# Optimization experiments

Hardware: AMD Instinct MI355X
Metric: run time of the kernel (lower is better)

The kernel has to match this reference:

```python
import jax, jax.numpy as jnp
import numpy as np

M_BITS = 4            # mem_pot_bits
M_MASK = (1 << M_BITS) - 1
T_MASK = (1 << 4) - 1  # t_bits = 4
ALPHA = 0.5


def setup_inputs() -> dict:
    key = jax.random.key(0)
    ks = jax.random.split(key, 8)
    B, N_IN, N_OUT, M = 256, 4096, 4096, 1 << M_BITS
    return {
        "active_mask": jax.random.randint(ks[0], (B, N_IN), 0, 2, dtype=jnp.int32),
        "t": 7,
        "prev_neuron_id": jax.random.randint(ks[1], (N_IN,), 0, M, dtype=jnp.int32),
        "t_last": jnp.zeros((B,), jnp.int32),
        "mem_fict": jax.random.uniform(ks[2], (B, N_OUT), jnp.float32),
        "mem_phys": jax.random.randint(ks[3], (B, N_OUT), 0, M, dtype=jnp.int32),
        "accumulate_lut_delta": jnp.zeros((N_OUT, M), jnp.float32),
        "tau": jax.random.uniform(ks[4], (N_OUT,), jnp.float32),
        "v_th": jax.random.uniform(ks[5], (N_OUT,), jnp.float32),
        "syn_w": jax.random.uniform(ks[6], (N_IN, N_OUT), jnp.float32),
        "mem_map": jax.nn.sigmoid(jax.random.normal(ks[7], (N_OUT, M), jnp.float32)),
    }


def reference(active_mask, t, prev_neuron_id, t_last, mem_fict, mem_phys,
              accumulate_lut_delta, tau, v_th, syn_w, mem_map):
    # delta_t = (t - t_last) & t_bit_mask  (Python '&' binds looser than '-')
    delta_t = (t - t_last) & T_MASK                          # (B,)
    t_last_new = jnp.full_like(t_last, t)

    # masked matmul + exponential membrane decay
    weights_sum = active_mask.astype(jnp.float32) @ syn_w    # (B, N_out)
    decay = jnp.exp(-tau[None, :] * delta_t[:, None].astype(jnp.float32))
    mem_fict_new = mem_fict * decay + weights_sum

    # XOR tree-reduction over masked input ids == bitwise parity per bit.
    # Only the low M_BITS matter (result is masked by m_bit_mask afterwards).
    masked_ids = jnp.where(active_mask.astype(bool), prev_neuron_id[None, :], 0)
    shifts = jnp.arange(M_BITS, dtype=jnp.int32)
    bits = (masked_ids[:, :, None] >> shifts) & 1            # (B, N_in, M_BITS)
    parity = jnp.sum(bits, axis=1) & 1                       # (B, M_BITS)
    acc = jnp.sum(parity << shifts, axis=1)                  # (B,)

    # physical membrane update (all low-bit integer ops)
    mem_phys_new = (mem_phys ^ delta_t[:, None] ^ acc[:, None]) & M_MASK

    # LUT gather + threshold
    n_out = mem_map.shape[0]
    rows = jnp.broadcast_to(jnp.arange(n_out)[None, :], mem_phys_new.shape)
    v_map_vals = mem_map[rows, mem_phys_new]                 # (B, N_out)
    active_next = v_map_vals >= v_th[None, :]

    # scatter-add per-bucket LUT delta (alpha != 0 path)
    delta = ALPHA * (mem_phys_new.astype(jnp.float32) - v_map_vals)
    lut_new = accumulate_lut_delta.at[rows, mem_phys_new].add(delta)

    return active_next, mem_fict_new, mem_phys_new, lut_new, t_last_new
```

## Files before the change

### kernel.cpp

```cpp
#include <hip/hip_runtime.h>

typedef __attribute__((ext_vector_type(8))) short short8;
typedef __attribute__((ext_vector_type(4))) float f32x4;
typedef unsigned int u32;

#define N_IN  4096
#define N_OUT 4096
#define NBAT  256

#define OUT_ACT   0
#define OUT_FICT  1048576
#define OUT_PHYS  2097152
#define OUT_LUT   3145728
#define OUT_TLAST 3211264

#define WS_MASK   0
#define WS_PART   2097152
#define WS_DTF    (WS_PART + 16777216)
#define WS_DXA    (WS_DTF + 1024)

#define BM 128
#define BN 64
#define BK 64
#define SPLITK 4
#define KCHUNK (N_IN / SPLITK)
#define NTK (KCHUNK / BK)

__device__ __forceinline__ unsigned f2bf(float f) {
  unsigned u = __float_as_uint(f);
  return (u + 0x7FFFu + ((u >> 16) & 1u)) >> 16;
}

__device__ __forceinline__ void gload16(const void* g, void* l) {
  __builtin_amdgcn_global_load_lds(
      (const __attribute__((address_space(1))) u32*)g,
      (__attribute__((address_space(3))) u32*)l, 16, 0, 0);
}

__global__ __launch_bounds__(256) void snn_pre(
    const int* __restrict__ mask, const int* __restrict__ t_ptr,
    const int* __restrict__ pid, const int* __restrict__ t_last,
    float* __restrict__ dtf_ws, int* __restrict__ dxa_ws,
    u32* __restrict__ maskws, float* __restrict__ out)
{
  const int b = blockIdx.x, tid = threadIdx.x;
  const int k0 = tid * 16;
  const int4* mp = (const int4*)(mask + (size_t)b * N_IN + k0);
  const int4* pp = (const int4*)(pid + k0);
  int x = 0;
  u32 wv[8];
#pragma unroll
  for (int q = 0; q < 4; ++q) {
    int4 m = mp[q];
    int4 id = pp[q];
    x ^= (m.x ? id.x : 0) ^ (m.y ? id.y : 0) ^ (m.z ? id.z : 0) ^ (m.w ? id.w : 0);
    wv[q * 2]     = (m.x ? 0x3F80u : 0u) | ((m.y ? 0x3F80u : 0u) << 16);
    wv[q * 2 + 1] = (m.z ? 0x3F80u : 0u) | ((m.w ? 0x3F80u : 0u) << 16);
  }
  {
    const int kt = tid >> 2;
    const int gg = (tid & 3) * 2;
    u32* base = maskws + (size_t)b * 2048 + kt * 32;
    int g0 = gg ^ (b & 7), g1 = (gg + 1) ^ (b & 7);
    uint4 v0; v0.x = wv[0]; v0.y = wv[1]; v0.z = wv[2]; v0.w = wv[3];
    uint4 v1; v1.x = wv[4]; v1.y = wv[5]; v1.z = wv[6]; v1.w = wv[7];
    *(uint4*)(base + g0 * 4) = v0;
    *(uint4*)(base + g1 * 4) = v1;
  }
  x ^= __shfl_xor(x, 32); x ^= __shfl_xor(x, 16); x ^= __shfl_xor(x, 8);
  x ^= __shfl_xor(x, 4);  x ^= __shfl_xor(x, 2);  x ^= __shfl_xor(x, 1);
  __shared__ int wx[4];
  if ((tid & 63) == 0) wx[tid >> 6] = x;
  __syncthreads();
  if (tid == 0) {
    int acc = wx[0] ^ wx[1] ^ wx[2] ^ wx[3];
    int tt = t_ptr[0];
    int dt = (tt - t_last[b]) & 15;
    dtf_ws[b] = (float)dt;
    dxa_ws[b] = dt ^ (acc & 15);
    out[OUT_TLAST + b] = (float)tt;
  }
}

__global__ __launch_bounds__(256) void snn_gemm(
    const char* __restrict__ maskws, const float* __restrict__ synw,
    float* __restrict__ part)
{
  __shared__ __align__(16) char ldsA[3][BM * BK * 2];
  __shared__ __align__(16) char ldsB[2][BN * BK * 2];

  const int tid = threadIdx.x;
  const int lane = tid & 63, wid = tid >> 6;
  const int l15 = lane & 15, l4 = lane >> 4;
  const int bmb = blockIdx.x * BM, bnb = blockIdx.y * BN;
  const int kcb = blockIdx.z * KCHUNK;
  const int wm = wid >> 1, wn = wid & 1;

  const char* a_gbase = maskws + (size_t)bmb * 8192 + (size_t)kcb * 2;
  const int b_n = tid & 63;
  const int b_kq = tid >> 6;
  const float* b_gbase = synw + (size_t)(kcb + b_kq * 16) * N_OUT + bnb + b_n;

  auto issueA = [&](int kt) {
    char* dbase = &ldsA[kt % 3][wid * 1024];
    const char* g0 = a_gbase + (size_t)(tid >> 3) * 8192 + kt * 128 + (tid & 7) * 16;
#pragma unroll
    for (int i = 0; i < 4; ++i)
      gload16(g0 + (size_t)i * (32 * 8192), dbase + i * 4096);
  };
  auto loadB = [&](int kt, float* bv) {
    const float* g = b_gbase + (size_t)kt * BK * N_OUT;
#pragma unroll
    for (int j = 0; j < 16; ++j) bv[j] = g[(size_t)j * N_OUT];
  };
  auto writeB = [&](const float* bv, int buf) {
    u32 w[8];
#pragma unroll
    for (int p = 0; p < 8; ++p) w[p] = f2bf(bv[2 * p]) | (f2bf(bv[2 * p + 1]) << 16);
    const int gb = b_kq * 2, s = b_n & 7;
    uint4 v0; v0.x = w[0]; v0.y = w[1]; v0.z = w[2]; v0.w = w[3];
    uint4 v1; v1.x = w[4]; v1.y = w[5]; v1.z = w[6]; v1.w = w[7];
    *(uint4*)(&ldsB[buf][b_n * 128 + ((gb ^ s) * 16)]) = v0;
    *(uint4*)(&ldsB[buf][b_n * 128 + (((gb + 1) ^ s) * 16)]) = v1;
  };

  f32x4 acc[4][2] = {};

  auto compute = [&](int abuf, int bbuf) {
#pragma unroll
    for (int kk = 0; kk < 2; ++kk) {
      const int g0 = kk * 4 + l4;
      short8 a[4], b[2];
#pragma unroll
      for (int mi = 0; mi < 4; ++mi) {
        int row = wm * 64 + mi * 16 + l15;
        a[mi] = *(const short8*)(&ldsA[abuf][row * 128 + ((g0 ^ (row & 7)) * 16)]);
      }
#pragma unroll
      for (int nj = 0; nj < 2; ++nj) {
        int col = wn * 32 + nj * 16 + l15;
        b[nj] = *(const short8*)(&ldsB[bbuf][col * 128 + ((g0 ^ (col & 7)) * 16)]);
      }
#pragma unroll
      for (int mi = 0; mi < 4; ++mi)
#pragma unroll
        for (int nj = 0; nj < 2; ++nj)
          acc[mi][nj] = __builtin_amdgcn_mfma_f32_16x16x32_bf16(a[mi], b[nj], acc[mi][nj], 0, 0, 0);
    }
  };

  float bvA[16], bvB[16];

  issueA(0);
  loadB(0, bvA);
  issueA(1);

#define BODY(KT, CURBV, NXTBV)                                   \
  {                                                              \
    if ((KT) + 1 < NTK) loadB((KT) + 1, NXTBV);                  \
    writeB(CURBV, (KT) & 1);  \
    __builtin_amdgcn_sched_barrier(0);                           \
    asm volatile("s_waitcnt lgkmcnt(0)" ::: "memory");           \
    __builtin_amdgcn_s_barrier();                                \
    __builtin_amdgcn_sched_barrier(0);                           \
    if ((KT) + 2 < NTK) issueA((KT) + 2);                        \
    compute((KT) % 3, (KT) & 1);                                 \
  }

  for (int kt = 0; kt < NTK; kt += 2) {
    BODY(kt, bvA, bvB);
    BODY(kt + 1, bvB, bvA);
  }
#undef BODY

  float* pb = part + (size_t)blockIdx.z * (NBAT * N_OUT);
#pragma unroll
  for (int mi = 0; mi < 4; ++mi)
#pragma unroll
    for (int nj = 0; nj < 2; ++nj) {
      const int o = bnb + wn * 32 + nj * 16 + l15;
#pragma unroll
      for (int r = 0; r < 4; ++r) {
        const int b = bmb + wm * 64 + mi * 16 + l4 * 4 + r;
        pb[(size_t)b * N_OUT + o] = acc[mi][nj][r];
      }
    }
}

__global__ __launch_bounds__(256) void snn_reduce(
    const float* __restrict__ part, const float* __restrict__ memf,
    const int* __restrict__ memp, const float* __restrict__ tau,
    const float* __restrict__ vth, const float* __restrict__ mem_map,
    const float* __restrict__ dtf_ws, const int* __restrict__ dxa_ws,
    float* __restrict__ out)
{
  const int flat = (blockIdx.x * 256 + threadIdx.x) * 4;
  const int b = flat >> 12, o = flat & 4095;
  const float4 p0 = *(const float4*)(part + flat);
  const float4 p1 = *(const float4*)(part + 1048576 + flat);
  const float4 p2 = *(const float4*)(part + 2097152 + flat);
  const float4 p3 = *(const float4*)(part + 3145728 + flat);
  float4 ws;
  ws.x = (p0.x + p1.x) + (p2.x + p3.x);
  ws.y = (p0.y + p1.y) + (p2.y + p3.y);
  ws.z = (p0.z + p1.z) + (p2.z + p3.z);
  ws.w = (p0.w + p1.w) + (p2.w + p3.w);
  const float dtf = dtf_ws[b];
  const int dxa = dxa_ws[b];
  const float4 mf = *(const float4*)(memf + flat);
  const int4  mp = *(const int4*)(memp + flat);
  const float4 tv = *(const float4*)(tau + o);
  const float4 vv = *(const float4*)(vth + o);
  float4 act, fict, phys;
#define DO(c, oi) { float d = __expf(-tv.c * dtf); fict.c = mf.c * d + ws.c; \
                    int mpn = (mp.c ^ dxa) & 15; phys.c = (float)mpn; \
                    act.c = (mem_map[(o + oi) * 16 + mpn] >= vv.c) ? 1.f : 0.f; }
  DO(x, 0) DO(y, 1) DO(z, 2) DO(w, 3)
#undef DO
  *(float4*)(out + OUT_ACT  + flat) = act;
  *(float4*)(out + OUT_FICT + flat) = fict;
  *(float4*)(out + OUT_PHYS + flat) = phys;
}

__global__ __launch_bounds__(256) void snn_lut(
    const int* __restrict__ memp, const int* __restrict__ dxa_ws,
    const float* __restrict__ mem_map, const float* __restrict__ lut_in,
    float* __restrict__ out)
{
  __shared__ int mp[NBAT * 16];
  __shared__ int dxs[NBAT];
  const int tid = threadIdx.x;
  const int o0 = blockIdx.x * 16;
#pragma unroll
  for (int i = 0; i < 16; ++i) {
    int b = i * 16 + (tid >> 4);
    int oj = tid & 15;
    mp[b * 16 + oj] = memp[(size_t)b * N_OUT + o0 + oj];
  }
  dxs[tid] = dxa_ws[tid];
  __syncthreads();
  const int o_l = tid >> 4, m = tid & 15;
  int cnt = 0;
#pragma unroll 8
  for (int b = 0; b < NBAT; ++b) {
    int v = (mp[b * 16 + o_l] ^ dxs[b]) & 15;
    cnt += (v == m);
  }
  const int o = o0 + o_l;
  const float vmap = mem_map[o * 16 + m];
  out[OUT_LUT + o * 16 + m] = lut_in[o * 16 + m] + 0.5f * ((float)m - vmap) * (float)cnt;
}

extern "C" void kernel_launch(void* const* d_in, const int* in_sizes, int n_in,
                              void* d_out, int out_size, void* d_ws, size_t ws_size,
                              hipStream_t stream)
{
  const int*   mask    = (const int*)d_in[0];
  const int*   t_ptr   = (const int*)d_in[1];
  const int*   pid     = (const int*)d_in[2];
  const int*   t_last  = (const int*)d_in[3];
  const float* memf    = (const float*)d_in[4];
  const int*   memp    = (const int*)d_in[5];
  const float* lut_in  = (const float*)d_in[6];
  const float* tau     = (const float*)d_in[7];
  const float* vth     = (const float*)d_in[8];
  const float* synw    = (const float*)d_in[9];
  const float* mem_map = (const float*)d_in[10];
  float* out = (float*)d_out;

  char* wsb = (char*)d_ws;
  u32*   maskws = (u32*)(wsb + WS_MASK);
  float* part   = (float*)(wsb + WS_PART);
  float* dtf_ws = (float*)(wsb + WS_DTF);
  int*   dxa_ws = (int*)(wsb + WS_DXA);

  snn_pre<<<NBAT, 256, 0, stream>>>(mask, t_ptr, pid, t_last, dtf_ws, dxa_ws, maskws, out);
  snn_gemm<<<dim3(NBAT / BM, N_OUT / BN, SPLITK), 256, 0, stream>>>(
      (const char*)maskws, synw, part);
  snn_reduce<<<(NBAT * N_OUT) / 1024, 256, 0, stream>>>(
      part, memf, memp, tau, vth, mem_map, dtf_ws, dxa_ws, out);
  snn_lut<<<NBAT, 256, 0, stream>>>(memp, dxa_ws, mem_map, lut_in, out);
}
```

Baseline: 50.85 us.

## Halve GEMM N-tile, remap blocks across XCDs, and deepen B-load pipeline

Shrinks the GEMM tile to BN=32, so each of the four waves owns a 32-row slice and the grid doubles to 1024 blocks on a flat 1D launch. Block IDs are remapped so consecutive IDs on each XCD share N-tiles, which is meant to improve L2 reuse of syn_w and the mask. The pipeline now keeps B loads two stages ahead with a partial vmcnt wait, and A uses double rather than triple buffering. In exchange, each block does less MFMA work per byte of A loaded, so A traffic doubles, and the out-of-range modulo loads issued on the last iterations are redundant.

```diff
diff --git a/kernel.cpp b/kernel.cpp
--- a/kernel.cpp
+++ b/kernel.cpp
@@ -20,7 +20,7 @@
 #define WS_DXA    (WS_DTF + 1024)
 
 #define BM 128
-#define BN 64
+#define BN 32
 #define BK 64
 #define SPLITK 4
 #define KCHUNK (N_IN / SPLITK)
@@ -86,23 +86,27 @@
     const char* __restrict__ maskws, const float* __restrict__ synw,
     float* __restrict__ part)
 {
-  __shared__ __align__(16) char ldsA[3][BM * BK * 2];
+  __shared__ __align__(16) char ldsA[2][BM * BK * 2];
   __shared__ __align__(16) char ldsB[2][BN * BK * 2];
 
   const int tid = threadIdx.x;
   const int lane = tid & 63, wid = tid >> 6;
   const int l15 = lane & 15, l4 = lane >> 4;
-  const int bmb = blockIdx.x * BM, bnb = blockIdx.y * BN;
-  const int kcb = blockIdx.z * KCHUNK;
-  const int wm = wid >> 1, wn = wid & 1;
+
+  const int bid = blockIdx.x;
+  const int sid = (bid & 7) * 128 + (bid >> 3);
+  const int nb = sid >> 3;
+  const int mb = (sid >> 2) & 1;
+  const int kc = sid & 3;
+  const int bmb = mb * BM, bnb = nb * BN, kcb = kc * KCHUNK;
 
   const char* a_gbase = maskws + (size_t)bmb * 8192 + (size_t)kcb * 2;
-  const int b_n = tid & 63;
-  const int b_kq = tid >> 6;
-  const float* b_gbase = synw + (size_t)(kcb + b_kq * 16) * N_OUT + bnb + b_n;
+  const int b_n = tid & 31;
+  const int b_ko = tid >> 5;
+  const float* b_gbase = synw + (size_t)(kcb + b_ko * 8) * N_OUT + bnb + b_n;
 
   auto issueA = [&](int kt) {
-    char* dbase = &ldsA[kt % 3][wid * 1024];
+    char* dbase = &ldsA[kt & 1][wid * 1024];
     const char* g0 = a_gbase + (size_t)(tid >> 3) * 8192 + kt * 128 + (tid & 7) * 16;
 #pragma unroll
     for (int i = 0; i < 4; ++i)
@@ -111,77 +115,74 @@
   auto loadB = [&](int kt, float* bv) {
     const float* g = b_gbase + (size_t)kt * BK * N_OUT;
 #pragma unroll
-    for (int j = 0; j < 16; ++j) bv[j] = g[(size_t)j * N_OUT];
+    for (int j = 0; j < 8; ++j) bv[j] = g[(size_t)j * N_OUT];
   };
   auto writeB = [&](const float* bv, int buf) {
-    u32 w[8];
-#pragma unroll
-    for (int p = 0; p < 8; ++p) w[p] = f2bf(bv[2 * p]) | (f2bf(bv[2 * p + 1]) << 16);
-    const int gb = b_kq * 2, s = b_n & 7;
-    uint4 v0; v0.x = w[0]; v0.y = w[1]; v0.z = w[2]; v0.w = w[3];
-    uint4 v1; v1.x = w[4]; v1.y = w[5]; v1.z = w[6]; v1.w = w[7];
-    *(uint4*)(&ldsB[buf][b_n * 128 + ((gb ^ s) * 16)]) = v0;
-    *(uint4*)(&ldsB[buf][b_n * 128 + (((gb + 1) ^ s) * 16)]) = v1;
-  };
-
-  f32x4 acc[4][2] = {};
-
-  auto compute = [&](int abuf, int bbuf) {
+    u32 w[4];
+#pragma unroll
+    for (int p = 0; p < 4; ++p) w[p] = f2bf(bv[2 * p]) | (f2bf(bv[2 * p + 1]) << 16);
+    uint4 v; v.x = w[0]; v.y = w[1]; v.z = w[2]; v.w = w[3];
+    *(uint4*)(&ldsB[buf][b_n * 128 + ((b_ko ^ (b_n & 7)) * 16)]) = v;
+  };
+
+  f32x4 acc[2][2] = {};
+
+  auto compute = [&](int buf) {
 #pragma unroll
     for (int kk = 0; kk < 2; ++kk) {
       const int g0 = kk * 4 + l4;
-      short8 a[4], b[2];
-#pragma unroll
-      for (int mi = 0; mi < 4; ++mi) {
-        int row = wm * 64 + mi * 16 + l15;
-        a[mi] = *(const short8*)(&ldsA[abuf][row * 128 + ((g0 ^ (row & 7)) * 16)]);
+      short8 a[2], b[2];
+#pragma unroll
+      for (int mi = 0; mi < 2; ++mi) {
+        int row = wid * 32 + mi * 16 + l15;
+        a[mi] = *(const short8*)(&ldsA[buf][row * 128 + ((g0 ^ (row & 7)) * 16)]);
       }
 #pragma unroll
       for (int nj = 0; nj < 2; ++nj) {
-        int col = wn * 32 + nj * 16 + l15;
-        b[nj] = *(const short8*)(&ldsB[bbuf][col * 128 + ((g0 ^ (col & 7)) * 16)]);
+        int col = nj * 16 + l15;
+        b[nj] = *(const short8*)(&ldsB[buf][col * 128 + ((g0 ^ (col & 7)) * 16)]);
       }
 #pragma unroll
-      for (int mi = 0; mi < 4; ++mi)
+      for (int mi = 0; mi < 2; ++mi)
 #pragma unroll
         for (int nj = 0; nj < 2; ++nj)
           acc[mi][nj] = __builtin_amdgcn_mfma_f32_16x16x32_bf16(a[mi], b[nj], acc[mi][nj], 0, 0, 0);
     }
   };
 
-  float bvA[16], bvB[16];
+  float bvA[8], bvB[8];
 
   issueA(0);
   loadB(0, bvA);
-  issueA(1);
-
-#define BODY(KT, CURBV, NXTBV)                                   \
-  {                                                              \
-    if ((KT) + 1 < NTK) loadB((KT) + 1, NXTBV);                  \
-    writeB(CURBV, (KT) & 1);  \
-    __builtin_amdgcn_sched_barrier(0);                           \
-    asm volatile("s_waitcnt lgkmcnt(0)" ::: "memory");           \
-    __builtin_amdgcn_s_barrier();                                \
-    __builtin_amdgcn_sched_barrier(0);                           \
-    if ((KT) + 2 < NTK) issueA((KT) + 2);                        \
-    compute((KT) % 3, (KT) & 1);                                 \
+  loadB(1, bvB);
+
+#define BODY(KT, CURBV)                                            \
+  {                                                                \
+    writeB(CURBV, (KT) & 1);                                       \
+    loadB(((KT) + 2) & 15, CURBV);                                 \
+    __builtin_amdgcn_sched_barrier(0);                             \
+    asm volatile("s_waitcnt vmcnt(8) lgkmcnt(0)" ::: "memory");    \
+    __builtin_amdgcn_s_barrier();                                  \
+    __builtin_amdgcn_sched_barrier(0);                             \
+    issueA(((KT) + 1) & 15);                                       \
+    compute((KT) & 1);                                             \
   }
 
   for (int kt = 0; kt < NTK; kt += 2) {
-    BODY(kt, bvA, bvB);
-    BODY(kt + 1, bvB, bvA);
+    BODY(kt, bvA);
+    BODY(kt + 1, bvB);
   }
 #undef BODY
 
-  float* pb = part + (size_t)blockIdx.z * (NBAT * N_OUT);
-#pragma unroll
-  for (int mi = 0; mi < 4; ++mi)
+  float* pb = part + (size_t)kc * (NBAT * N_OUT);
+#pragma unroll
+  for (int mi = 0; mi < 2; ++mi)
 #pragma unroll
     for (int nj = 0; nj < 2; ++nj) {
-      const int o = bnb + wn * 32 + nj * 16 + l15;
+      const int o = bnb + nj * 16 + l15;
 #pragma unroll
       for (int r = 0; r < 4; ++r) {
-        const int b = bmb + wm * 64 + mi * 16 + l4 * 4 + r;
+        const int b = bmb + wid * 32 + mi * 16 + l4 * 4 + r;
         pb[(size_t)b * N_OUT + o] = acc[mi][nj][r];
       }
     }
@@ -275,7 +276,7 @@
   int*   dxa_ws = (int*)(wsb + WS_DXA);
 
   snn_pre<<<NBAT, 256, 0, stream>>>(mask, t_ptr, pid, t_last, dtf_ws, dxa_ws, maskws, out);
-  snn_gemm<<<dim3(NBAT / BM, N_OUT / BN, SPLITK), 256, 0, stream>>>(
+  snn_gemm<<<(NBAT / BM) * (N_OUT / BN) * SPLITK, 256, 0, stream>>>(
       (const char*)maskws, synw, part);
   snn_reduce<<<(NBAT * N_OUT) / 1024, 256, 0, stream>>>(
       part, memf, memp, tau, vth, mem_map, dtf_ws, dxa_ws, out);
```

New measurement: 48.20 us. -5.2%, faster.
